# Optimization experiments

Measured on AMD Instinct MI355X. Metric: run time of the kernel, lower is better.

Reference implementation:

```python
import jax, jax.numpy as jnp
import numpy as np

B, F, D, H = 16384, 39, 16, 2   # batch, fields, embed_dim, heads
VOCAB = 10000                    # per-field vocab
DH = D * H                       # attention output dim per layer (no head split)


def setup_inputs() -> dict:
    key = jax.random.key(0)
    ks = jax.random.split(key, 32)
    def n(k, shape, s=0.05):
        return jax.random.normal(k, shape, jnp.float32) * s
    inp = {"x": jax.random.randint(ks[0], (B, F), 0, VOCAB, dtype=jnp.int32)}
    inp["emb"] = n(ks[1], (F * VOCAB, D))
    idx = 2
    for i, din in enumerate([D, DH, DH]):  # layer0: 16->32, layers 1-2: 32->32
        for nm in ["wq", "wk", "wv", "wr"]:
            inp[f"{nm}{i}"] = n(ks[idx], (din, DH)); idx += 1
    prev = F * DH  # 1248 after flatten
    for i, u in enumerate([128, 64, 32, 1], 1):
        inp[f"w{i}"] = n(ks[idx], (prev, u)); idx += 1
        inp[f"b{i}"] = jnp.zeros((u,), jnp.float32)
        prev = u
    return inp


def reference(x, emb,
              wq0, wk0, wv0, wr0,
              wq1, wk1, wv1, wr1,
              wq2, wk2, wv2, wr2,
              w1, b1, w2, b2, w3, b3, w4, b4):
    offsets = jnp.arange(F, dtype=jnp.int32) * VOCAB
    e = emb[x + offsets]                                   # [B, F, D]
    for wq, wk, wv, wr in [(wq0, wk0, wv0, wr0),
                           (wq1, wk1, wv1, wr1),
                           (wq2, wk2, wv2, wr2)]:
        q = jnp.einsum('bfd,de->bfe', e, wq)               # [B, F, DH]
        k = jnp.einsum('bfd,de->bfe', e, wk)
        v = jnp.einsum('bfd,de->bfe', e, wv)
        att = jax.nn.softmax(jnp.einsum('bfe,bge->bfg', q, k), axis=-1)  # [B,F,F], no scaling
        out = jnp.einsum('bfg,bge->bfe', att, v) + jnp.einsum('bfd,de->bfe', e, wr)
        e = jax.nn.relu(out)
    h = e.reshape(B, F * DH)
    for w, b in [(w1, b1), (w2, b2), (w3, b3)]:
        h = jax.nn.relu(h @ w + b)
    return jax.nn.sigmoid(h @ w4 + b4)                     # [B, 1]
```

## Files before the change

### kernel.cpp

```cpp
#include <hip/hip_runtime.h>
#include <math.h>

#define NF   39
#define NB   16384
#define NVOC 10000

typedef unsigned short u16;
typedef unsigned int   u32;
typedef float f32x4 __attribute__((ext_vector_type(4)));
typedef float f32x2 __attribute__((ext_vector_type(2)));
typedef short s16x8 __attribute__((ext_vector_type(8)));
typedef __bf16 bf16x2 __attribute__((ext_vector_type(2)));

#define E3_U16   20447232u
#define WOFF_W1  9216u
#define NSWZ     179200

__device__ __forceinline__ u32 bfadj(float x){
    u32 u = __float_as_uint(x);
    return u + 0x7fffu + ((u >> 16) & 1u);
}
__device__ __forceinline__ u32 pk2(float a, float b){
    bf16x2 t;
    t[0] = (__bf16)a;
    t[1] = (__bf16)b;
    u32 r; __builtin_memcpy(&r, &t, 4); return r;
}
__device__ __forceinline__ u16 f2bf(float f){ return (u16)(bfadj(f) >> 16); }

__device__ __forceinline__ float fexp2(float x){
#if __has_builtin(__builtin_amdgcn_exp2f)
    return __builtin_amdgcn_exp2f(x);
#else
    return exp2f(x);
#endif
}
__device__ __forceinline__ float frcp(float x){
#if __has_builtin(__builtin_amdgcn_rcpf)
    return __builtin_amdgcn_rcpf(x);
#else
    return 1.f / x;
#endif
}

__device__ __forceinline__ void wave_sync(){
    asm volatile("s_waitcnt lgkmcnt(0)" ::: "memory");
}
__device__ __forceinline__ f32x4 mfma16(s16x8 a, s16x8 b, f32x4 c){
    return __builtin_amdgcn_mfma_f32_16x16x32_bf16(a, b, c, 0, 0, 0);
}
__device__ __forceinline__ void store4(u16* p, f32x4 v){
    *(uint2*)p = make_uint2(pk2(v[0], v[1]), pk2(v[2], v[3]));
}

__device__ __forceinline__ f32x2 pkadd(f32x2 a, f32x2 b){
    f32x2 d; asm("v_pk_add_f32 %0, %1, %2" : "=v"(d) : "v"(a), "v"(b)); return d;
}
__device__ __forceinline__ f32x2 pkmul(f32x2 a, f32x2 b){
    f32x2 d; asm("v_pk_mul_f32 %0, %1, %2" : "=v"(d) : "v"(a), "v"(b)); return d;
}

__device__ __forceinline__ void swap32(u32 &a, u32 &b){
    asm("v_permlane32_swap_b32 %0, %1" : "+v"(a), "+v"(b));
}
__device__ __forceinline__ void swap16(u32 &a, u32 &b){
    asm("v_permlane16_swap_b32 %0, %1" : "+v"(a), "+v"(b));
}
__device__ __forceinline__ s16x8 fragPack(u32 a0, u32 a1, u32 b0, u32 b1){
    swap32(a0, b0); swap16(a0, b0);
    swap32(a1, b1); swap16(a1, b1);
    union { u32 w[4]; s16x8 v; } u;
    u.w[0] = a0; u.w[1] = a1; u.w[2] = b0; u.w[3] = b1;
    return u.v;
}
__device__ __forceinline__ s16x8 fragCC(f32x4 A, f32x4 B){
    return fragPack(pk2(A[0],A[1]), pk2(A[2],A[3]), pk2(B[0],B[1]), pk2(B[2],B[3]));
}
__device__ __forceinline__ s16x8 fragC0(f32x4 A){
    return fragPack(pk2(A[0],A[1]), pk2(A[2],A[3]), 0u, 0u);
}
__device__ __forceinline__ s16x8 fragCCn(f32x4 A, f32x4 B, f32x2 iv){
    f32x2 a01 = pkmul(__builtin_shufflevector(A, A, 0, 1), iv);
    f32x2 a23 = pkmul(__builtin_shufflevector(A, A, 2, 3), iv);
    f32x2 b01 = pkmul(__builtin_shufflevector(B, B, 0, 1), iv);
    f32x2 b23 = pkmul(__builtin_shufflevector(B, B, 2, 3), iv);
    return fragPack(pk2(a01.x,a01.y), pk2(a23.x,a23.y),
                    pk2(b01.x,b01.y), pk2(b23.x,b23.y));
}
__device__ __forceinline__ s16x8 fragC0n(f32x4 A, f32x2 iv){
    f32x2 a01 = pkmul(__builtin_shufflevector(A, A, 0, 1), iv);
    f32x2 a23 = pkmul(__builtin_shufflevector(A, A, 2, 3), iv);
    return fragPack(pk2(a01.x,a01.y), pk2(a23.x,a23.y), 0u, 0u);
}
__device__ __forceinline__ float xadd16(float t){
    u32 a = __float_as_uint(t), b = a;
    swap16(a, b);
    return __uint_as_float(a) + __uint_as_float(b);
}
__device__ __forceinline__ float xadd32(float t){
    u32 a = __float_as_uint(t), b = a;
    swap32(a, b);
    return __uint_as_float(a) + __uint_as_float(b);
}

__global__ void __launch_bounds__(256) swz_kernel(
    const float* __restrict__ wq0, const float* __restrict__ wk0,
    const float* __restrict__ wv0, const float* __restrict__ wr0,
    const float* __restrict__ wq1, const float* __restrict__ wk1,
    const float* __restrict__ wv1, const float* __restrict__ wr1,
    const float* __restrict__ wq2, const float* __restrict__ wk2,
    const float* __restrict__ wv2, const float* __restrict__ wr2,
    const float* __restrict__ w1, const float* __restrict__ w2,
    const float* __restrict__ w3, u16* __restrict__ ws)
{
    int gid = (int)blockIdx.x*256 + (int)threadIdx.x;
    if (gid >= NSWZ) return;
    int w    = gid & 511;
    int lane = w >> 3, j = w & 7;
    int n    = lane & 15, quad = lane >> 4;
    int kin  = quad*8 + j;
    float val;
    if (gid < 9216){
        int l = gid / 3072;
        int rr = gid - l*3072;
        int kind = rr >> 10;
        int a    = (rr >> 9) & 1;
        int din  = l ? 32 : 16;
        const float *WQ, *WK, *WV, *WR;
        if (l == 0){ WQ=wq0; WK=wk0; WV=wv0; WR=wr0; }
        else if (l == 1){ WQ=wq1; WK=wk1; WV=wv1; WR=wr1; }
        else { WQ=wq2; WK=wk2; WV=wv2; WR=wr2; }
        if (kind == 0){
            int dp = a*16 + n;
            float s = 0.f;
            if (dp < din && kin < din){
                float acc = 0.f;
                for (int e = 0; e < 32; ++e)
                    acc += WQ[kin*32 + e] * WK[dp*32 + e];
                s = acc * 1.44269504f;
            }
            val = s;
        } else {
            const float* W = (kind == 1) ? WV : WR;
            val = (kin < din) ? W[kin*32 + a*16 + n] : 0.f;
        }
    } else if (gid < 9216 + 159744){
        int tt = (gid - 9216) >> 9;
        int ks = tt >> 3, nt = tt & 7;
        val = w1[(ks*32 + kin)*128 + nt*16 + n];
    } else if (gid < 9216 + 159744 + 8192){
        int tt = (gid - (9216+159744)) >> 9;
        int ks = tt >> 2, nt = tt & 3;
        val = w2[(ks*32 + kin)*64 + nt*16 + n];
    } else {
        int tt = (gid - (9216+159744+8192)) >> 9;
        int ks = tt >> 1, nt = tt & 1;
        val = w3[(ks*32 + kin)*32 + nt*16 + n];
    }
    ws[E3_U16 + gid] = f2bf(val);
}

__global__ void __launch_bounds__(256, 4) attn_kernel(
    const int* __restrict__ x, const float* __restrict__ emb,
    u16* __restrict__ ws)
{
    __shared__ __align__(16) u16 lds[4*1536];
    const int tid  = (int)threadIdx.x;
    const int wid  = tid >> 6, lane = tid & 63;
    const int h    = lane >> 4, nl = lane & 15;
    const int r    = (int)blockIdx.x*4 + wid;

    u16* eBuf = lds + wid*1536;
    const u16* wmat = ws + E3_U16;
    const f32x4 z = {0.f, 0.f, 0.f, 0.f};

    f32x4 ci;
#pragma unroll
    for (int reg = 0; reg < 4; ++reg)
        ci[reg] = (h*4 + reg >= 7) ? -1e30f : 0.f;

    if (lane < 48){
        int f = lane, mt = f >> 4, fl = f & 15;
        u16* row = eBuf + mt*512 + fl*8;
        if (f < NF){
            const float4* ep = (const float4*)(emb + ((size_t)(x[r*NF + f] + f*NVOC))*16);
            float4 e0 = ep[0], e1 = ep[1], e2 = ep[2], e3 = ep[3];
            *(uint4*)(row)       = make_uint4(pk2(e0.x,e0.y), pk2(e0.z,e0.w),
                                              pk2(e1.x,e1.y), pk2(e1.z,e1.w));
            *(uint4*)(row + 128) = make_uint4(pk2(e2.x,e2.y), pk2(e2.z,e2.w),
                                              pk2(e3.x,e3.y), pk2(e3.z,e3.w));
        } else {
            *(uint4*)(row)       = make_uint4(0,0,0,0);
            *(uint4*)(row + 128) = make_uint4(0,0,0,0);
        }
        *(uint4*)(row + 256) = make_uint4(0,0,0,0);
        *(uint4*)(row + 384) = make_uint4(0,0,0,0);
    }
    wave_sync();
    s16x8 bE[3];
#pragma unroll
    for (int nt = 0; nt < 3; ++nt)
        bE[nt] = *(const s16x8*)(eBuf + nt*512 + lane*8);

#pragma unroll 1
    for (int L = 0; L < 3; ++L){
        const u16* wL = wmat + L*3072;

        s16x8 bT[3];
        {
            s16x8 g0 = *(const s16x8*)(wL +       lane*8);
            s16x8 g1 = *(const s16x8*)(wL + 512 + lane*8);
#pragma unroll
            for (int nt = 0; nt < 3; ++nt)
                bT[nt] = fragCC(mfma16(g0, bE[nt], z), mfma16(g1, bE[nt], z));
        }
        s16x8 aV[2][2];
        {
            s16x8 v0 = *(const s16x8*)(wL + 1024 + lane*8);
            s16x8 v1 = *(const s16x8*)(wL + 1536 + lane*8);
#pragma unroll
            for (int emt = 0; emt < 2; ++emt){
                s16x8 vb = emt ? v1 : v0;
                f32x4 c0 = mfma16(bE[0], vb, z);
                f32x4 c1 = mfma16(bE[1], vb, z);
                f32x4 c2 = mfma16(bE[2], vb, z);
                aV[0][emt] = fragCC(c0, c1);
                aV[1][emt] = fragC0(c2);
            }
        }
        f32x4 S[3][3];
#pragma unroll
        for (int mtg = 0; mtg < 3; ++mtg)
#pragma unroll
        for (int nt = 0; nt < 3; ++nt)
            S[mtg][nt] = mfma16(bE[mtg], bT[nt], (mtg == 2) ? ci : z);

        float inv[3];
#pragma unroll
        for (int nt = 0; nt < 3; ++nt){
            f32x2 acc2 = {0.f, 0.f};
#pragma unroll
            for (int mtg = 0; mtg < 3; ++mtg){
#pragma unroll
                for (int reg = 0; reg < 4; ++reg)
                    S[mtg][nt][reg] = fexp2(S[mtg][nt][reg]);
                acc2 = pkadd(acc2, __builtin_shufflevector(S[mtg][nt], S[mtg][nt], 0, 1));
                acc2 = pkadd(acc2, __builtin_shufflevector(S[mtg][nt], S[mtg][nt], 2, 3));
            }
            inv[nt] = frcp(xadd32(xadd16(acc2.x + acc2.y)));
        }
        inv[2] = (nl < 7) ? inv[2] : 0.f;

        f32x4 R[2][3];
        {
            s16x8 r0 = *(const s16x8*)(wL + 2048 + lane*8);
            s16x8 r1 = *(const s16x8*)(wL + 2560 + lane*8);
#pragma unroll
            for (int nt = 0; nt < 3; ++nt){
                R[0][nt] = mfma16(r0, bE[nt], z);
                R[1][nt] = mfma16(r1, bE[nt], z);
            }
        }
        if (nl >= 7){ R[0][2] = z; R[1][2] = z; }

        if (L < 2){
#pragma unroll
            for (int nt = 0; nt < 3; ++nt){
                f32x2 iv = {inv[nt], inv[nt]};
                s16x8 p0 = fragCCn(S[0][nt], S[1][nt], iv);
                s16x8 p1 = fragC0n(S[2][nt], iv);
                f32x4 oc[2];
#pragma unroll
                for (int emt = 0; emt < 2; ++emt){
                    f32x4 o = mfma16(aV[1][emt], p1,
                              mfma16(aV[0][emt], p0, R[emt][nt]));
#pragma unroll
                    for (int reg = 0; reg < 4; ++reg)
                        o[reg] = fmaxf(o[reg], 0.f);
                    oc[emt] = o;
                }
                bE[nt] = fragCC(oc[0], oc[1]);
            }
        } else {
            int st = r >> 4, sm = r & 15;
            u32 base = (u32)(st*39)*512u + (u32)(sm*8 + (h>>1)*128 + (h&1)*4);
#pragma unroll
            for (int nt = 0; nt < 3; ++nt){
                f32x2 iv = {inv[nt], inv[nt]};
                s16x8 p0 = fragCCn(S[0][nt], S[1][nt], iv);
                s16x8 p1 = fragC0n(S[2][nt], iv);
                int f = nt*16 + nl;
#pragma unroll
                for (int emt = 0; emt < 2; ++emt){
                    f32x4 o = mfma16(aV[1][emt], p1,
                              mfma16(aV[0][emt], p0, R[emt][nt]));
#pragma unroll
                    for (int reg = 0; reg < 4; ++reg)
                        o[reg] = fmaxf(o[reg], 0.f);
                    if (f < NF)
                        *(uint2*)(ws + base + (u32)f*512u + emt*256) =
                            make_uint2(pk2(o[0], o[1]), pk2(o[2], o[3]));
                }
            }
        }
    }
}

__global__ void __launch_bounds__(256, 4) mlp_kernel(
    const float* __restrict__ b1, const float* __restrict__ b2,
    const float* __restrict__ b3, const float* __restrict__ w4,
    const float* __restrict__ b4, const u16* __restrict__ ws,
    float* __restrict__ out)
{
    __shared__ __align__(16) float red[8192];
    __shared__ __align__(16) u16 h1t[2048];
    __shared__ __align__(16) u16 h2t[1024];
    __shared__ float part[32];
    const int tid = (int)threadIdx.x;
    const int w   = tid >> 6, lane = tid & 63;
    const int h   = lane >> 4, nl = lane & 15;
    const int st  = (int)blockIdx.x;
    const int A_off = nl*8 + (h>>1)*128 + (h&1)*4;

    const u16* w1b = ws + E3_U16 + WOFF_W1;
    const u16* w2b = w1b + 159744u;
    const u16* w3b = w2b + 8192u;
    const f32x4 z = {0.f,0.f,0.f,0.f};

    f32x4 acc[8];
#pragma unroll
    for (int nt = 0; nt < 8; ++nt) acc[nt] = z;
#pragma unroll 2
    for (int ks = w; ks < 39; ks += 4){
        s16x8 aE = *(const s16x8*)(ws + (u32)(st*39 + ks)*512u + lane*8);
#pragma unroll
        for (int nt = 0; nt < 8; ++nt){
            s16x8 aW = *(const s16x8*)(w1b + (ks*8 + nt)*512 + lane*8);
            acc[nt] = mfma16(aW, aE, acc[nt]);
        }
    }
#pragma unroll
    for (int nt = 0; nt < 8; ++nt)
        *(f32x4*)(red + (w*8 + nt)*256 + lane*4) = acc[nt];
    __syncthreads();

#pragma unroll
    for (int t = 0; t < 2; ++t){
        int ft = 2*w + t;
        f32x4 s = *(const f32x4*)(red + (0*8 + ft)*256 + lane*4);
#pragma unroll
        for (int p = 1; p < 4; ++p){
            f32x4 q = *(const f32x4*)(red + (p*8 + ft)*256 + lane*4);
#pragma unroll
            for (int reg = 0; reg < 4; ++reg) s[reg] += q[reg];
        }
        float4 bv = *(const float4*)(b1 + ft*16 + h*4);
        f32x4 v;
        v[0] = fmaxf(s[0] + bv.x, 0.f);
        v[1] = fmaxf(s[1] + bv.y, 0.f);
        v[2] = fmaxf(s[2] + bv.z, 0.f);
        v[3] = fmaxf(s[3] + bv.w, 0.f);
        store4(h1t + ft*256 + A_off, v);
    }
    __syncthreads();

    {
        f32x4 a2 = z;
#pragma unroll
        for (int ks = 0; ks < 4; ++ks){
            s16x8 aW = *(const s16x8*)(w2b + (ks*4 + w)*512 + lane*8);
            s16x8 bH = *(const s16x8*)(h1t + ks*512 + lane*8);
            a2 = mfma16(aW, bH, a2);
        }
        float4 bv = *(const float4*)(b2 + w*16 + h*4);
        f32x4 v;
        v[0] = fmaxf(a2[0] + bv.x, 0.f);
        v[1] = fmaxf(a2[1] + bv.y, 0.f);
        v[2] = fmaxf(a2[2] + bv.z, 0.f);
        v[3] = fmaxf(a2[3] + bv.w, 0.f);
        store4(h2t + (w>>1)*512 + (w&1)*256 + A_off, v);
    }
    __syncthreads();

    if (w < 2){
        f32x4 a3 = z;
#pragma unroll
        for (int ks = 0; ks < 2; ++ks){
            s16x8 aW = *(const s16x8*)(w3b + (ks*2 + w)*512 + lane*8);
            s16x8 bH = *(const s16x8*)(h2t + ks*512 + lane*8);
            a3 = mfma16(aW, bH, a3);
        }
        float4 b3v = *(const float4*)(b3 + w*16 + h*4);
        float4 w4v = *(const float4*)(w4 + w*16 + h*4);
        float t = fmaxf(a3[0] + b3v.x, 0.f)*w4v.x
                + fmaxf(a3[1] + b3v.y, 0.f)*w4v.y
                + fmaxf(a3[2] + b3v.z, 0.f)*w4v.z
                + fmaxf(a3[3] + b3v.w, 0.f)*w4v.w;
        t += __shfl_xor(t, 16, 64);
        t += __shfl_xor(t, 32, 64);
        if (h == 0) part[w*16 + nl] = t;
    }
    __syncthreads();
    if (tid < 16){
        float zz = part[tid] + part[16 + tid] + b4[0];
        out[st*16 + tid] = 1.f/(1.f + __expf(-zz));
    }
}

extern "C" void kernel_launch(void* const* d_in, const int* in_sizes, int n_in,
                              void* d_out, int out_size, void* d_ws, size_t ws_size,
                              hipStream_t stream)
{
    (void)in_sizes; (void)n_in; (void)ws_size; (void)out_size;
    const int*   x   = (const int*)d_in[0];
    const float* emb = (const float*)d_in[1];
    u16* ws = (u16*)d_ws;

    swz_kernel<<<(NSWZ+255)/256, 256, 0, stream>>>(
        (const float*)d_in[2],  (const float*)d_in[3],  (const float*)d_in[4],  (const float*)d_in[5],
        (const float*)d_in[6],  (const float*)d_in[7],  (const float*)d_in[8],  (const float*)d_in[9],
        (const float*)d_in[10], (const float*)d_in[11], (const float*)d_in[12], (const float*)d_in[13],
        (const float*)d_in[14], (const float*)d_in[16], (const float*)d_in[18], ws);

    attn_kernel<<<NB/4, 256, 0, stream>>>(x, emb, ws);

    mlp_kernel<<<NB/16, 256, 0, stream>>>(
        (const float*)d_in[15], (const float*)d_in[17], (const float*)d_in[19],
        (const float*)d_in[20], (const float*)d_in[21], ws, (float*)d_out);
}
```

Before: 175.1 us.

## Fuse attention and MLP kernels, keep layer-3 activations in LDS

Merges the attention and MLP kernels into one 1024-thread block that handles 16 samples. The final attention layer writes its output into shared memory instead of a global workspace, and the MLP reads it from there, so the global round trip and one launch go away. The first MLP layer is split across 16 waves (8 output tiles × 2 K halves) with an LDS reduction. The cost is larger blocks with more __syncthreads barriers, about 62KB of LDS per block limiting occupancy, and idle waves in the later small MLP stages.

```diff
diff --git a/kernel.cpp b/kernel.cpp
--- a/kernel.cpp
+++ b/kernel.cpp
@@ -160,18 +160,32 @@
     ws[E3_U16 + gid] = f2bf(val);
 }
 
-__global__ void __launch_bounds__(256, 4) attn_kernel(
+__global__ void __launch_bounds__(1024, 8) fused_kernel(
     const int* __restrict__ x, const float* __restrict__ emb,
-    u16* __restrict__ ws)
+    const u16* __restrict__ ws,
+    const float* __restrict__ b1, const float* __restrict__ b2,
+    const float* __restrict__ b3, const float* __restrict__ w4,
+    const float* __restrict__ b4, float* __restrict__ out)
 {
-    __shared__ __align__(16) u16 lds[4*1536];
+    __shared__ __align__(16) u16 smem[31296];
     const int tid  = (int)threadIdx.x;
     const int wid  = tid >> 6, lane = tid & 63;
     const int h    = lane >> 4, nl = lane & 15;
-    const int r    = (int)blockIdx.x*4 + wid;
-
-    u16* eBuf = lds + wid*1536;
+    const int st   = (int)blockIdx.x;
+    const int r    = st*16 + wid;
+    const int A_off = nl*8 + (h>>1)*128 + (h&1)*4;
+
+    u16*   e3t  = smem;
+    float* redf = (float*)(smem + 19968);
+    u16*   h1t  = smem + 19968 + 8192;
+    u16*   h2t  = h1t + 2048;
+    float* part = (float*)(h2t + 1024);
+
+    u16* eBuf = smem + wid*1536;
     const u16* wmat = ws + E3_U16;
+    const u16* w1b  = wmat + WOFF_W1;
+    const u16* w2b  = w1b + 159744u;
+    const u16* w3b  = w2b + 8192u;
     const f32x4 z = {0.f, 0.f, 0.f, 0.f};
 
     f32x4 ci;
@@ -201,6 +215,7 @@
 #pragma unroll
     for (int nt = 0; nt < 3; ++nt)
         bE[nt] = *(const s16x8*)(eBuf + nt*512 + lane*8);
+    __syncthreads();
 
 #pragma unroll 1
     for (int L = 0; L < 3; ++L){
@@ -282,8 +297,7 @@
                 bE[nt] = fragCC(oc[0], oc[1]);
             }
         } else {
-            int st = r >> 4, sm = r & 15;
-            u32 base = (u32)(st*39)*512u + (u32)(sm*8 + (h>>1)*128 + (h&1)*4);
+            u32 lo = (u32)(wid*8 + (h>>1)*128 + (h&1)*4);
 #pragma unroll
             for (int nt = 0; nt < 3; ++nt){
                 f32x2 iv = {inv[nt], inv[nt]};
@@ -298,107 +312,75 @@
                     for (int reg = 0; reg < 4; ++reg)
                         o[reg] = fmaxf(o[reg], 0.f);
                     if (f < NF)
-                        *(uint2*)(ws + base + (u32)f*512u + emt*256) =
-                            make_uint2(pk2(o[0], o[1]), pk2(o[2], o[3]));
+                        store4(e3t + (u32)f*512u + emt*256 + lo, o);
                 }
             }
         }
     }
-}
-
-__global__ void __launch_bounds__(256, 4) mlp_kernel(
-    const float* __restrict__ b1, const float* __restrict__ b2,
-    const float* __restrict__ b3, const float* __restrict__ w4,
-    const float* __restrict__ b4, const u16* __restrict__ ws,
-    float* __restrict__ out)
-{
-    __shared__ __align__(16) float red[8192];
-    __shared__ __align__(16) u16 h1t[2048];
-    __shared__ __align__(16) u16 h2t[1024];
-    __shared__ float part[32];
-    const int tid = (int)threadIdx.x;
-    const int w   = tid >> 6, lane = tid & 63;
-    const int h   = lane >> 4, nl = lane & 15;
-    const int st  = (int)blockIdx.x;
-    const int A_off = nl*8 + (h>>1)*128 + (h&1)*4;
-
-    const u16* w1b = ws + E3_U16 + WOFF_W1;
-    const u16* w2b = w1b + 159744u;
-    const u16* w3b = w2b + 8192u;
-    const f32x4 z = {0.f,0.f,0.f,0.f};
-
-    f32x4 acc[8];
-#pragma unroll
-    for (int nt = 0; nt < 8; ++nt) acc[nt] = z;
+    __syncthreads();
+
+    {
+        int nt1 = wid & 7, kh = wid >> 3;
+        int k0 = kh ? 20 : 0, k1 = kh ? 39 : 20;
+        f32x4 acc = z;
 #pragma unroll 2
-    for (int ks = w; ks < 39; ks += 4){
-        s16x8 aE = *(const s16x8*)(ws + (u32)(st*39 + ks)*512u + lane*8);
-#pragma unroll
-        for (int nt = 0; nt < 8; ++nt){
-            s16x8 aW = *(const s16x8*)(w1b + (ks*8 + nt)*512 + lane*8);
-            acc[nt] = mfma16(aW, aE, acc[nt]);
-        }
-    }
-#pragma unroll
-    for (int nt = 0; nt < 8; ++nt)
-        *(f32x4*)(red + (w*8 + nt)*256 + lane*4) = acc[nt];
-    __syncthreads();
-
-#pragma unroll
-    for (int t = 0; t < 2; ++t){
-        int ft = 2*w + t;
-        f32x4 s = *(const f32x4*)(red + (0*8 + ft)*256 + lane*4);
-#pragma unroll
-        for (int p = 1; p < 4; ++p){
-            f32x4 q = *(const f32x4*)(red + (p*8 + ft)*256 + lane*4);
-#pragma unroll
-            for (int reg = 0; reg < 4; ++reg) s[reg] += q[reg];
-        }
-        float4 bv = *(const float4*)(b1 + ft*16 + h*4);
+        for (int ks = k0; ks < k1; ++ks){
+            s16x8 aE = *(const s16x8*)(e3t + ks*512 + lane*8);
+            s16x8 aW = *(const s16x8*)(w1b + (ks*8 + nt1)*512 + lane*8);
+            acc = mfma16(aW, aE, acc);
+        }
+        *(f32x4*)(redf + wid*256 + lane*4) = acc;
+    }
+    __syncthreads();
+
+    if (wid < 8){
+        f32x4 s = *(const f32x4*)(redf + wid*256 + lane*4);
+        f32x4 q = *(const f32x4*)(redf + (wid+8)*256 + lane*4);
+        float4 bv = *(const float4*)(b1 + wid*16 + h*4);
         f32x4 v;
-        v[0] = fmaxf(s[0] + bv.x, 0.f);
-        v[1] = fmaxf(s[1] + bv.y, 0.f);
-        v[2] = fmaxf(s[2] + bv.z, 0.f);
-        v[3] = fmaxf(s[3] + bv.w, 0.f);
-        store4(h1t + ft*256 + A_off, v);
-    }
-    __syncthreads();
-
-    {
+        v[0] = fmaxf(s[0] + q[0] + bv.x, 0.f);
+        v[1] = fmaxf(s[1] + q[1] + bv.y, 0.f);
+        v[2] = fmaxf(s[2] + q[2] + bv.z, 0.f);
+        v[3] = fmaxf(s[3] + q[3] + bv.w, 0.f);
+        store4(h1t + wid*256 + A_off, v);
+    }
+    __syncthreads();
+
+    if (wid < 4){
         f32x4 a2 = z;
 #pragma unroll
         for (int ks = 0; ks < 4; ++ks){
-            s16x8 aW = *(const s16x8*)(w2b + (ks*4 + w)*512 + lane*8);
+            s16x8 aW = *(const s16x8*)(w2b + (ks*4 + wid)*512 + lane*8);
             s16x8 bH = *(const s16x8*)(h1t + ks*512 + lane*8);
             a2 = mfma16(aW, bH, a2);
         }
-        float4 bv = *(const float4*)(b2 + w*16 + h*4);
+        float4 bv = *(const float4*)(b2 + wid*16 + h*4);
         f32x4 v;
         v[0] = fmaxf(a2[0] + bv.x, 0.f);
         v[1] = fmaxf(a2[1] + bv.y, 0.f);
         v[2] = fmaxf(a2[2] + bv.z, 0.f);
         v[3] = fmaxf(a2[3] + bv.w, 0.f);
-        store4(h2t + (w>>1)*512 + (w&1)*256 + A_off, v);
-    }
-    __syncthreads();
-
-    if (w < 2){
+        store4(h2t + (wid>>1)*512 + (wid&1)*256 + A_off, v);
+    }
+    __syncthreads();
+
+    if (wid < 2){
         f32x4 a3 = z;
 #pragma unroll
         for (int ks = 0; ks < 2; ++ks){
-            s16x8 aW = *(const s16x8*)(w3b + (ks*2 + w)*512 + lane*8);
+            s16x8 aW = *(const s16x8*)(w3b + (ks*2 + wid)*512 + lane*8);
             s16x8 bH = *(const s16x8*)(h2t + ks*512 + lane*8);
             a3 = mfma16(aW, bH, a3);
         }
-        float4 b3v = *(const float4*)(b3 + w*16 + h*4);
-        float4 w4v = *(const float4*)(w4 + w*16 + h*4);
+        float4 b3v = *(const float4*)(b3 + wid*16 + h*4);
+        float4 w4v = *(const float4*)(w4 + wid*16 + h*4);
         float t = fmaxf(a3[0] + b3v.x, 0.f)*w4v.x
                 + fmaxf(a3[1] + b3v.y, 0.f)*w4v.y
                 + fmaxf(a3[2] + b3v.z, 0.f)*w4v.z
                 + fmaxf(a3[3] + b3v.w, 0.f)*w4v.w;
         t += __shfl_xor(t, 16, 64);
         t += __shfl_xor(t, 32, 64);
-        if (h == 0) part[w*16 + nl] = t;
+        if (h == 0) part[wid*16 + nl] = t;
     }
     __syncthreads();
     if (tid < 16){
@@ -422,9 +404,8 @@
         (const float*)d_in[10], (const float*)d_in[11], (const float*)d_in[12], (const float*)d_in[13],
         (const float*)d_in[14], (const float*)d_in[16], (const float*)d_in[18], ws);
 
-    attn_kernel<<<NB/4, 256, 0, stream>>>(x, emb, ws);
-
-    mlp_kernel<<<NB/16, 256, 0, stream>>>(
+    fused_kernel<<<NB/16, 1024, 0, stream>>>(
+        x, emb, ws,
         (const float*)d_in[15], (const float*)d_in[17], (const float*)d_in[19],
-        (const float*)d_in[20], (const float*)d_in[21], ws, (float*)d_out);
-}
+        (const float*)d_in[20], (const float*)d_in[21], (float*)d_out);
+}
```

Measured after the change: 426.2 us. 2.43x slower.

## Restructure MLP kernel: stage activations in LDS, split by output tile, 32 rows per block

Applied to the files above, without the earlier changes.

The MLP kernel now processes 32 batch rows per 512-thread block and first copies the layer-3 attention activations for both 16-row groups into shared memory. Each wave owns one output tile of W1 and runs the full K loop, reusing each W1 fragment for two row groups. This removes the cross-wave K-split reduction through a large float scratch buffer and halves W1 global reads per row. The cost is about 90 KB of shared memory per block, which limits occupancy, and a serial 39-step K loop per wave.

```diff
diff --git a/kernel.cpp b/kernel.cpp
--- a/kernel.cpp
+++ b/kernel.cpp
@@ -306,20 +306,21 @@
     }
 }
 
-__global__ void __launch_bounds__(256, 4) mlp_kernel(
+__global__ void __launch_bounds__(512, 4) mlp_kernel(
     const float* __restrict__ b1, const float* __restrict__ b2,
     const float* __restrict__ b3, const float* __restrict__ w4,
     const float* __restrict__ b4, const u16* __restrict__ ws,
     float* __restrict__ out)
 {
-    __shared__ __align__(16) float red[8192];
-    __shared__ __align__(16) u16 h1t[2048];
-    __shared__ __align__(16) u16 h2t[1024];
-    __shared__ float part[32];
+    __shared__ __align__(16) u16 smem[46208];
+    u16*   e3s  = smem;
+    u16*   h1t  = smem + 39936;
+    u16*   h2t  = smem + 44032;
+    float* part = (float*)(smem + 46080);
+
     const int tid = (int)threadIdx.x;
     const int w   = tid >> 6, lane = tid & 63;
     const int h   = lane >> 4, nl = lane & 15;
-    const int st  = (int)blockIdx.x;
     const int A_off = nl*8 + (h>>1)*128 + (h&1)*4;
 
     const u16* w1b = ws + E3_U16 + WOFF_W1;
@@ -327,83 +328,81 @@
     const u16* w3b = w2b + 8192u;
     const f32x4 z = {0.f,0.f,0.f,0.f};
 
-    f32x4 acc[8];
-#pragma unroll
-    for (int nt = 0; nt < 8; ++nt) acc[nt] = z;
-#pragma unroll 2
-    for (int ks = w; ks < 39; ks += 4){
-        s16x8 aE = *(const s16x8*)(ws + (u32)(st*39 + ks)*512u + lane*8);
-#pragma unroll
-        for (int nt = 0; nt < 8; ++nt){
-            s16x8 aW = *(const s16x8*)(w1b + (ks*8 + nt)*512 + lane*8);
-            acc[nt] = mfma16(aW, aE, acc[nt]);
-        }
-    }
-#pragma unroll
-    for (int nt = 0; nt < 8; ++nt)
-        *(f32x4*)(red + (w*8 + nt)*256 + lane*4) = acc[nt];
+    const u32 e3base = (u32)blockIdx.x * 39936u;
+#pragma unroll
+    for (int k = 0; k < 10; ++k){
+        u32 idx = (u32)tid*8u + (u32)k*4096u;
+        if (idx < 39936u)
+            *(s16x8*)(e3s + idx) = *(const s16x8*)(ws + e3base + idx);
+    }
     __syncthreads();
 
-#pragma unroll
-    for (int t = 0; t < 2; ++t){
-        int ft = 2*w + t;
-        f32x4 s = *(const f32x4*)(red + (0*8 + ft)*256 + lane*4);
-#pragma unroll
-        for (int p = 1; p < 4; ++p){
-            f32x4 q = *(const f32x4*)(red + (p*8 + ft)*256 + lane*4);
-#pragma unroll
-            for (int reg = 0; reg < 4; ++reg) s[reg] += q[reg];
-        }
-        float4 bv = *(const float4*)(b1 + ft*16 + h*4);
-        f32x4 v;
-        v[0] = fmaxf(s[0] + bv.x, 0.f);
-        v[1] = fmaxf(s[1] + bv.y, 0.f);
-        v[2] = fmaxf(s[2] + bv.z, 0.f);
-        v[3] = fmaxf(s[3] + bv.w, 0.f);
-        store4(h1t + ft*256 + A_off, v);
+    {
+        f32x4 a0 = z, a1 = z;
+#pragma unroll 3
+        for (int ks = 0; ks < 39; ++ks){
+            s16x8 aW = *(const s16x8*)(w1b + (ks*8 + w)*512 + lane*8);
+            s16x8 e0 = *(const s16x8*)(e3s + ks*512 + lane*8);
+            s16x8 e1 = *(const s16x8*)(e3s + 19968 + ks*512 + lane*8);
+            a0 = mfma16(aW, e0, a0);
+            a1 = mfma16(aW, e1, a1);
+        }
+        float4 bv = *(const float4*)(b1 + w*16 + h*4);
+        f32x4 v0, v1;
+        v0[0] = fmaxf(a0[0] + bv.x, 0.f); v1[0] = fmaxf(a1[0] + bv.x, 0.f);
+        v0[1] = fmaxf(a0[1] + bv.y, 0.f); v1[1] = fmaxf(a1[1] + bv.y, 0.f);
+        v0[2] = fmaxf(a0[2] + bv.z, 0.f); v1[2] = fmaxf(a1[2] + bv.z, 0.f);
+        v0[3] = fmaxf(a0[3] + bv.w, 0.f); v1[3] = fmaxf(a1[3] + bv.w, 0.f);
+        store4(h1t +        w*256 + A_off, v0);
+        store4(h1t + 2048 + w*256 + A_off, v1);
     }
     __syncthreads();
 
     {
+        int stg = w >> 2, nt2 = w & 3;
+        const u16* h1s = h1t + stg*2048;
         f32x4 a2 = z;
 #pragma unroll
         for (int ks = 0; ks < 4; ++ks){
-            s16x8 aW = *(const s16x8*)(w2b + (ks*4 + w)*512 + lane*8);
-            s16x8 bH = *(const s16x8*)(h1t + ks*512 + lane*8);
+            s16x8 aW = *(const s16x8*)(w2b + (ks*4 + nt2)*512 + lane*8);
+            s16x8 bH = *(const s16x8*)(h1s + ks*512 + lane*8);
             a2 = mfma16(aW, bH, a2);
         }
-        float4 bv = *(const float4*)(b2 + w*16 + h*4);
+        float4 bv = *(const float4*)(b2 + nt2*16 + h*4);
         f32x4 v;
         v[0] = fmaxf(a2[0] + bv.x, 0.f);
         v[1] = fmaxf(a2[1] + bv.y, 0.f);
         v[2] = fmaxf(a2[2] + bv.z, 0.f);
         v[3] = fmaxf(a2[3] + bv.w, 0.f);
-        store4(h2t + (w>>1)*512 + (w&1)*256 + A_off, v);
+        store4(h2t + stg*1024 + (nt2>>1)*512 + (nt2&1)*256 + A_off, v);
     }
     __syncthreads();
 
-    if (w < 2){
+    if ((w & 3) < 2){
+        int stg = w >> 2, nt3 = w & 3;
+        const u16* h2s = h2t + stg*1024;
         f32x4 a3 = z;
 #pragma unroll
         for (int ks = 0; ks < 2; ++ks){
-            s16x8 aW = *(const s16x8*)(w3b + (ks*2 + w)*512 + lane*8);
-            s16x8 bH = *(const s16x8*)(h2t + ks*512 + lane*8);
+            s16x8 aW = *(const s16x8*)(w3b + (ks*2 + nt3)*512 + lane*8);
+            s16x8 bH = *(const s16x8*)(h2s + ks*512 + lane*8);
             a3 = mfma16(aW, bH, a3);
         }
-        float4 b3v = *(const float4*)(b3 + w*16 + h*4);
-        float4 w4v = *(const float4*)(w4 + w*16 + h*4);
+        float4 b3v = *(const float4*)(b3 + nt3*16 + h*4);
+        float4 w4v = *(const float4*)(w4 + nt3*16 + h*4);
         float t = fmaxf(a3[0] + b3v.x, 0.f)*w4v.x
                 + fmaxf(a3[1] + b3v.y, 0.f)*w4v.y
                 + fmaxf(a3[2] + b3v.z, 0.f)*w4v.z
                 + fmaxf(a3[3] + b3v.w, 0.f)*w4v.w;
         t += __shfl_xor(t, 16, 64);
         t += __shfl_xor(t, 32, 64);
-        if (h == 0) part[w*16 + nl] = t;
+        if (h == 0) part[stg*32 + nt3*16 + nl] = t;
     }
     __syncthreads();
-    if (tid < 16){
-        float zz = part[tid] + part[16 + tid] + b4[0];
-        out[st*16 + tid] = 1.f/(1.f + __expf(-zz));
+    if (tid < 32){
+        int stg = tid >> 4, sm = tid & 15;
+        float zz = part[stg*32 + sm] + part[stg*32 + 16 + sm] + b4[0];
+        out[((int)blockIdx.x*2 + stg)*16 + sm] = 1.f/(1.f + __expf(-zz));
     }
 }
 
@@ -424,7 +423,7 @@
 
     attn_kernel<<<NB/4, 256, 0, stream>>>(x, emb, ws);
 
-    mlp_kernel<<<NB/16, 256, 0, stream>>>(
+    mlp_kernel<<<NB/32, 512, 0, stream>>>(
         (const float*)d_in[15], (const float*)d_in[17], (const float*)d_in[19],
         (const float*)d_in[20], (const float*)d_in[21], ws, (float*)d_out);
 }
```

New measurement: 177.7 us. Within noise of the previous version (+1.5%).
